# Kernel optimization log

Measured on AMD Instinct MI355X. Metric: run time of the kernel, lower is better.

Reference implementation:

```python
import jax, jax.numpy as jnp
import numpy as np


def _l2_normalize(x):
    # matches features.div(features.norm(2, 1, keepdim=True))
    return x / jnp.linalg.norm(x, ord=2, axis=1, keepdims=True)


def setup_inputs() -> dict:
    key = jax.random.key(0)
    k1, k2, k3 = jax.random.split(key, 3)
    B, N, D, C = 2048, 100000, 512, 1000
    return {
        "features": jax.random.normal(k1, (B, D), dtype=jnp.float32),
        "logits": jax.random.normal(k2, (B, C), dtype=jnp.float32),
        "db_features": jax.random.normal(k3, (N, D), dtype=jnp.float32),
        "k": 10,
    }


def reference(features, logits, db_features, k):
    # fit(): index.add(normalize(db_features)) -- faiss IndexFlatL2 stores rows
    xb = _l2_normalize(db_features)            # [N, D]
    # forward(): search normalized queries, take k-th (largest of the k) squared L2 dist
    xq = _l2_normalize(features)               # [B, D]
    # squared L2 distances via the expansion ||q||^2 + ||x||^2 - 2 q.x (faiss IndexFlatL2
    # returns SQUARED distances)
    q2 = jnp.sum(xq * xq, axis=1, keepdims=True)           # [B, 1]
    x2 = jnp.sum(xb * xb, axis=1)                          # [N]
    d2 = q2 + x2[None, :] - 2.0 * (xq @ xb.T)              # [B, N]
    # k smallest distances == k largest of -d2
    neg_topk, _ = jax.lax.top_k(-d2, k)                    # [B, k], sorted descending
    kth = -neg_topk[:, -1]                                 # k-th nearest squared distance
    return kth.reshape(-1, 1)
```

## Files before the change

### kernel.cpp

```cpp
#include <hip/hip_runtime.h>
#include <hip/hip_bf16.h>

typedef unsigned short ushort_t;
typedef unsigned char uchar_t;
typedef __attribute__((ext_vector_type(4))) int int4v;
typedef __attribute__((ext_vector_type(2))) unsigned int uint2v;

#define NQ      2048
#define ND      512
#define NDB     100000
#define TOPK    10
#define NCHUNK  98
#define CHUNK_N 1024
#define NPAD    (NCHUNK * CHUNK_N)
#define QTILES  (NQ / 128)
#define NTILES  (CHUNK_N / 128)
#define NWG     (NCHUNK * QTILES)
#define PERXCD  (NWG / 8)
#define QSCALE  400.0f
#define QINV    (1.0f / (QSCALE * QSCALE))
#define IMIN    (-2147483647 - 1)

#define GL2LDS(gp, lp) __builtin_amdgcn_global_load_lds(                      \
    (const __attribute__((address_space(1))) void*)(gp),                     \
    (__attribute__((address_space(3))) void*)(lp), 16, 0, 0)

__global__ void normalize_rows_i8(const float* __restrict__ in, uchar_t* __restrict__ out,
                                  int nvalid, int ntotal) {
    int row  = blockIdx.x * 4 + (threadIdx.x >> 6);
    int lane = threadIdx.x & 63;
    if (row >= ntotal) return;
    uint2v pk;
    if (row >= nvalid) {
        pk[0] = 0u; pk[1] = 0u;
    } else {
        const float4* src = reinterpret_cast<const float4*>(in + (size_t)row * ND);
        float4 v0 = src[lane * 2];
        float4 v1 = src[lane * 2 + 1];
        float s = v0.x*v0.x + v0.y*v0.y + v0.z*v0.z + v0.w*v0.w
                + v1.x*v1.x + v1.y*v1.y + v1.z*v1.z + v1.w*v1.w;
        #pragma unroll
        for (int off = 32; off; off >>= 1) s += __shfl_xor(s, off, 64);
        float r = rsqrtf(s) * QSCALE;
        float f[8] = { v0.x, v0.y, v0.z, v0.w, v1.x, v1.y, v1.z, v1.w };
        unsigned b[8];
        #pragma unroll
        for (int i = 0; i < 8; ++i) {
            int q = (int)rintf(f[i] * r);
            q = q > 127 ? 127 : (q < -127 ? -127 : q);
            b[i] = (unsigned)q & 0xFFu;
        }
        pk[0] = b[0] | (b[1] << 8) | (b[2] << 16) | (b[3] << 24);
        pk[1] = b[4] | (b[5] << 8) | (b[6] << 16) | (b[7] << 24);
    }
    *reinterpret_cast<uint2v*>(out + (size_t)row * ND + lane * 8) = pk;
}

__device__ inline void topk_insert_i(int (&top)[TOPK], int x) {
    #pragma unroll
    for (int i = 0; i < TOPK; ++i) {
        int mx = top[i] > x ? top[i] : x;
        int mn = top[i] > x ? x : top[i];
        top[i] = mx;
        x = mn;
    }
}

__global__ __launch_bounds__(256, 4)
void knn_chunk(const uchar_t* __restrict__ qb, const uchar_t* __restrict__ dbb,
               int* __restrict__ partial) {
    const int logical = (blockIdx.x & 7) * PERXCD + (blockIdx.x >> 3);
    const int qt = logical & (QTILES - 1);
    const int nc = logical >> 4;
    const int t = threadIdx.x, lane = t & 63, wv = t >> 6;

    __shared__ __align__(16) uchar_t As[128 * 64];
    __shared__ __align__(16) uchar_t Bs[128 * 64];

    int top[2][TOPK];
    #pragma unroll
    for (int qs = 0; qs < 2; ++qs)
        #pragma unroll
        for (int i = 0; i < TOPK; ++i) top[qs][i] = IMIN;

    const size_t nchunkbase = (size_t)nc * CHUNK_N;
    const int cb = wv * 128;
    const uchar_t* aseg = qb + (size_t)(qt * 128) * ND;

    int soff[2], doff[2];
    #pragma unroll
    for (int i = 0; i < 2; ++i) {
        const int cid = cb + i * 64 + lane;
        const int row = cid >> 2;
        const int c   = (cid & 3) ^ ((row >> 1) & 3);
        soff[i] = row * ND + c * 16;
        doff[i] = cid * 16;
    }
    const int cgrp = lane >> 4;
    int aoff[2];
    #pragma unroll
    for (int qs = 0; qs < 2; ++qs) {
        const int ar = wv * 32 + qs * 16 + (lane & 15);
        aoff[qs] = ar * 64 + ((cgrp ^ ((ar >> 1) & 3)) * 16);
    }
    int boff[8];
    #pragma unroll
    for (int ns = 0; ns < 8; ++ns) {
        const int br = ns * 16 + (lane & 15);
        boff[ns] = br * 64 + ((cgrp ^ ((br >> 1) & 3)) * 16);
    }

    for (int nt = 0; nt < NTILES; ++nt) {
        const uchar_t* bseg = dbb + (nchunkbase + nt * 128) * ND;
        int4v acc[2][8];
        #pragma unroll
        for (int a = 0; a < 2; ++a)
            #pragma unroll
            for (int b = 0; b < 8; ++b)
                acc[a][b] = (int4v){0, 0, 0, 0};

        #pragma unroll
        for (int ks = 0; ks < 8; ++ks) {
            const int kbase = ks * 64;
            __syncthreads();
            #pragma unroll
            for (int i = 0; i < 2; ++i) {
                GL2LDS(aseg + soff[i] + kbase, As + doff[i]);
                GL2LDS(bseg + soff[i] + kbase, Bs + doff[i]);
            }
            __syncthreads();
            int4v af[2], bf[8];
            #pragma unroll
            for (int qs = 0; qs < 2; ++qs)
                af[qs] = *reinterpret_cast<const int4v*>(As + aoff[qs]);
            #pragma unroll
            for (int ns = 0; ns < 8; ++ns)
                bf[ns] = *reinterpret_cast<const int4v*>(Bs + boff[ns]);
            #pragma unroll
            for (int qs = 0; qs < 2; ++qs)
                #pragma unroll
                for (int ns = 0; ns < 8; ++ns)
                    acc[qs][ns] = __builtin_amdgcn_mfma_i32_16x16x64_i8(bf[ns], af[qs], acc[qs][ns], 0, 0, 0);
        }

        #pragma unroll
        for (int qs = 0; qs < 2; ++qs) {
            int m = acc[qs][0][0];
            #pragma unroll
            for (int ns = 0; ns < 8; ++ns)
                #pragma unroll
                for (int r = 0; r < 4; ++r)
                    m = m > acc[qs][ns][r] ? m : acc[qs][ns][r];
            if (m > top[qs][TOPK - 1]) {
                #pragma unroll
                for (int ns = 0; ns < 8; ++ns)
                    #pragma unroll
                    for (int r = 0; r < 4; ++r) {
                        int v = acc[qs][ns][r];
                        if (v > top[qs][TOPK - 1]) topk_insert_i(top[qs], v);
                    }
            }
        }
    }

    #pragma unroll
    for (int qs = 0; qs < 2; ++qs) {
        #pragma unroll
        for (int step = 16; step <= 32; step <<= 1) {
            int other[TOPK];
            #pragma unroll
            for (int i = 0; i < TOPK; ++i) other[i] = __shfl_xor(top[qs][i], step, 64);
            #pragma unroll
            for (int i = 0; i < TOPK; ++i)
                if (other[i] > top[qs][TOPK - 1]) topk_insert_i(top[qs], other[i]);
        }
    }

    if ((lane >> 4) == 0) {
        #pragma unroll
        for (int qs = 0; qs < 2; ++qs) {
            const int q = qt * 128 + wv * 32 + qs * 16 + lane;
            int* dst = partial + ((size_t)nc * NQ + q) * TOPK;
            #pragma unroll
            for (int i = 0; i < TOPK; ++i) dst[i] = top[qs][i];
        }
    }
}

__global__ void final_merge(const int* __restrict__ partial, float* __restrict__ out) {
    const int q = blockIdx.x * 4 + (threadIdx.x >> 6);
    const int lane = threadIdx.x & 63;
    if (q >= NQ) return;
    int top[TOPK];
    #pragma unroll
    for (int i = 0; i < TOPK; ++i) top[i] = IMIN;
    for (int c = lane; c < NCHUNK; c += 64) {
        const int* p = partial + ((size_t)c * NQ + q) * TOPK;
        #pragma unroll
        for (int i = 0; i < TOPK; ++i) {
            int x = p[i];
            if (x > top[TOPK - 1]) topk_insert_i(top, x);
        }
    }
    #pragma unroll
    for (int step = 1; step <= 32; step <<= 1) {
        int other[TOPK];
        #pragma unroll
        for (int i = 0; i < TOPK; ++i) other[i] = __shfl_xor(top[i], step, 64);
        #pragma unroll
        for (int i = 0; i < TOPK; ++i)
            if (other[i] > top[TOPK - 1]) topk_insert_i(top, other[i]);
    }
    if (lane == 0) out[q] = 2.0f - 2.0f * ((float)top[TOPK - 1] * QINV);
}

extern "C" void kernel_launch(void* const* d_in, const int* in_sizes, int n_in,
                              void* d_out, int out_size, void* d_ws, size_t ws_size,
                              hipStream_t stream) {
    const float* features = (const float*)d_in[0];
    const float* dbf      = (const float*)d_in[2];
    float* out = (float*)d_out;

    uchar_t* dbb = (uchar_t*)d_ws;
    uchar_t* qbn = dbb + (size_t)NPAD * ND;
    int* partial = (int*)(qbn + (size_t)NQ * ND);

    normalize_rows_i8<<<NPAD / 4, 256, 0, stream>>>(dbf, dbb, NDB, NPAD);
    normalize_rows_i8<<<NQ / 4, 256, 0, stream>>>(features, qbn, NQ, NQ);
    knn_chunk<<<NWG, 256, 0, stream>>>(qbn, dbb, partial);
    final_merge<<<NQ / 4, 256, 0, stream>>>(partial, out);
}
```

Baseline: 327.1 us.

## Split knn tile across 8 waves, one 16-query slab per wave

```diff
diff --git a/kernel.cpp b/kernel.cpp
--- a/kernel.cpp
+++ b/kernel.cpp
@@ -66,124 +66,102 @@
     }
 }
 
-__global__ __launch_bounds__(256, 4)
+__global__ __launch_bounds__(512, 8)
 void knn_chunk(const uchar_t* __restrict__ qb, const uchar_t* __restrict__ dbb,
                int* __restrict__ partial) {
     const int logical = (blockIdx.x & 7) * PERXCD + (blockIdx.x >> 3);
     const int qt = logical & (QTILES - 1);
     const int nc = logical >> 4;
     const int t = threadIdx.x, lane = t & 63, wv = t >> 6;
+    const int l15 = lane & 15;
 
     __shared__ __align__(16) uchar_t As[128 * 64];
     __shared__ __align__(16) uchar_t Bs[128 * 64];
 
-    int top[2][TOPK];
-    #pragma unroll
-    for (int qs = 0; qs < 2; ++qs)
-        #pragma unroll
-        for (int i = 0; i < TOPK; ++i) top[qs][i] = IMIN;
+    int top[TOPK];
+    #pragma unroll
+    for (int i = 0; i < TOPK; ++i) top[i] = IMIN;
 
     const size_t nchunkbase = (size_t)nc * CHUNK_N;
-    const int cb = wv * 128;
     const uchar_t* aseg = qb + (size_t)(qt * 128) * ND;
 
-    int soff[2], doff[2];
-    #pragma unroll
-    for (int i = 0; i < 2; ++i) {
-        const int cid = cb + i * 64 + lane;
-        const int row = cid >> 2;
-        const int c   = (cid & 3) ^ ((row >> 1) & 3);
-        soff[i] = row * ND + c * 16;
-        doff[i] = cid * 16;
-    }
+    const int srow = t >> 2;
+    const int scol = (t & 3) ^ ((srow >> 1) & 3);
+    const int soff = srow * ND + scol * 16;
+    const int doff = t * 16;
     const int cgrp = lane >> 4;
-    int aoff[2];
-    #pragma unroll
-    for (int qs = 0; qs < 2; ++qs) {
-        const int ar = wv * 32 + qs * 16 + (lane & 15);
-        aoff[qs] = ar * 64 + ((cgrp ^ ((ar >> 1) & 3)) * 16);
-    }
-    int boff[8];
-    #pragma unroll
-    for (int ns = 0; ns < 8; ++ns) {
-        const int br = ns * 16 + (lane & 15);
-        boff[ns] = br * 64 + ((cgrp ^ ((br >> 1) & 3)) * 16);
-    }
+    const int slot = (cgrp ^ ((l15 >> 1) & 3)) * 16;
+    const int aoff = (wv * 16 + l15) * 64 + slot;
+    const int boff = l15 * 64 + slot;
 
     for (int nt = 0; nt < NTILES; ++nt) {
         const uchar_t* bseg = dbb + (nchunkbase + nt * 128) * ND;
-        int4v acc[2][8];
-        #pragma unroll
-        for (int a = 0; a < 2; ++a)
-            #pragma unroll
-            for (int b = 0; b < 8; ++b)
-                acc[a][b] = (int4v){0, 0, 0, 0};
+        int4v acc[8];
+        #pragma unroll
+        for (int b = 0; b < 8; ++b) acc[b] = (int4v){0, 0, 0, 0};
 
         #pragma unroll
         for (int ks = 0; ks < 8; ++ks) {
             const int kbase = ks * 64;
             __syncthreads();
+            GL2LDS(aseg + soff + kbase, As + doff);
+            GL2LDS(bseg + soff + kbase, Bs + doff);
+            __syncthreads();
+            int4v af = *reinterpret_cast<const int4v*>(As + aoff);
+            {
+                int4v bf0 = *reinterpret_cast<const int4v*>(Bs + boff);
+                int4v bf1 = *reinterpret_cast<const int4v*>(Bs + boff + 1024);
+                int4v bf2 = *reinterpret_cast<const int4v*>(Bs + boff + 2048);
+                int4v bf3 = *reinterpret_cast<const int4v*>(Bs + boff + 3072);
+                acc[0] = __builtin_amdgcn_mfma_i32_16x16x64_i8(bf0, af, acc[0], 0, 0, 0);
+                acc[1] = __builtin_amdgcn_mfma_i32_16x16x64_i8(bf1, af, acc[1], 0, 0, 0);
+                acc[2] = __builtin_amdgcn_mfma_i32_16x16x64_i8(bf2, af, acc[2], 0, 0, 0);
+                acc[3] = __builtin_amdgcn_mfma_i32_16x16x64_i8(bf3, af, acc[3], 0, 0, 0);
+            }
+            {
+                int4v bf4 = *reinterpret_cast<const int4v*>(Bs + boff + 4096);
+                int4v bf5 = *reinterpret_cast<const int4v*>(Bs + boff + 5120);
+                int4v bf6 = *reinterpret_cast<const int4v*>(Bs + boff + 6144);
+                int4v bf7 = *reinterpret_cast<const int4v*>(Bs + boff + 7168);
+                acc[4] = __builtin_amdgcn_mfma_i32_16x16x64_i8(bf4, af, acc[4], 0, 0, 0);
+                acc[5] = __builtin_amdgcn_mfma_i32_16x16x64_i8(bf5, af, acc[5], 0, 0, 0);
+                acc[6] = __builtin_amdgcn_mfma_i32_16x16x64_i8(bf6, af, acc[6], 0, 0, 0);
+                acc[7] = __builtin_amdgcn_mfma_i32_16x16x64_i8(bf7, af, acc[7], 0, 0, 0);
+            }
+        }
+
+        int m = acc[0][0];
+        #pragma unroll
+        for (int ns = 0; ns < 8; ++ns)
             #pragma unroll
-            for (int i = 0; i < 2; ++i) {
-                GL2LDS(aseg + soff[i] + kbase, As + doff[i]);
-                GL2LDS(bseg + soff[i] + kbase, Bs + doff[i]);
-            }
-            __syncthreads();
-            int4v af[2], bf[8];
-            #pragma unroll
-            for (int qs = 0; qs < 2; ++qs)
-                af[qs] = *reinterpret_cast<const int4v*>(As + aoff[qs]);
-            #pragma unroll
-            for (int ns = 0; ns < 8; ++ns)
-                bf[ns] = *reinterpret_cast<const int4v*>(Bs + boff[ns]);
-            #pragma unroll
-            for (int qs = 0; qs < 2; ++qs)
-                #pragma unroll
-                for (int ns = 0; ns < 8; ++ns)
-                    acc[qs][ns] = __builtin_amdgcn_mfma_i32_16x16x64_i8(bf[ns], af[qs], acc[qs][ns], 0, 0, 0);
-        }
-
-        #pragma unroll
-        for (int qs = 0; qs < 2; ++qs) {
-            int m = acc[qs][0][0];
+            for (int r = 0; r < 4; ++r)
+                m = m > acc[ns][r] ? m : acc[ns][r];
+        if (m > top[TOPK - 1]) {
             #pragma unroll
             for (int ns = 0; ns < 8; ++ns)
                 #pragma unroll
-                for (int r = 0; r < 4; ++r)
-                    m = m > acc[qs][ns][r] ? m : acc[qs][ns][r];
-            if (m > top[qs][TOPK - 1]) {
-                #pragma unroll
-                for (int ns = 0; ns < 8; ++ns)
-                    #pragma unroll
-                    for (int r = 0; r < 4; ++r) {
-                        int v = acc[qs][ns][r];
-                        if (v > top[qs][TOPK - 1]) topk_insert_i(top[qs], v);
-                    }
-            }
-        }
-    }
-
-    #pragma unroll
-    for (int qs = 0; qs < 2; ++qs) {
-        #pragma unroll
-        for (int step = 16; step <= 32; step <<= 1) {
-            int other[TOPK];
-            #pragma unroll
-            for (int i = 0; i < TOPK; ++i) other[i] = __shfl_xor(top[qs][i], step, 64);
-            #pragma unroll
-            for (int i = 0; i < TOPK; ++i)
-                if (other[i] > top[qs][TOPK - 1]) topk_insert_i(top[qs], other[i]);
-        }
+                for (int r = 0; r < 4; ++r) {
+                    int v = acc[ns][r];
+                    if (v > top[TOPK - 1]) topk_insert_i(top, v);
+                }
+        }
+    }
+
+    #pragma unroll
+    for (int step = 16; step <= 32; step <<= 1) {
+        int other[TOPK];
+        #pragma unroll
+        for (int i = 0; i < TOPK; ++i) other[i] = __shfl_xor(top[i], step, 64);
+        #pragma unroll
+        for (int i = 0; i < TOPK; ++i)
+            if (other[i] > top[TOPK - 1]) topk_insert_i(top, other[i]);
     }
 
     if ((lane >> 4) == 0) {
-        #pragma unroll
-        for (int qs = 0; qs < 2; ++qs) {
-            const int q = qt * 128 + wv * 32 + qs * 16 + lane;
-            int* dst = partial + ((size_t)nc * NQ + q) * TOPK;
-            #pragma unroll
-            for (int i = 0; i < TOPK; ++i) dst[i] = top[qs][i];
-        }
+        const int q = qt * 128 + wv * 16 + l15;
+        int* dst = partial + ((size_t)nc * NQ + q) * TOPK;
+        #pragma unroll
+        for (int i = 0; i < TOPK; ++i) dst[i] = top[i];
     }
 }
 
@@ -227,6 +205,6 @@
 
     normalize_rows_i8<<<NPAD / 4, 256, 0, stream>>>(dbf, dbb, NDB, NPAD);
     normalize_rows_i8<<<NQ / 4, 256, 0, stream>>>(features, qbn, NQ, NQ);
-    knn_chunk<<<NWG, 256, 0, stream>>>(qbn, dbb, partial);
+    knn_chunk<<<NWG, 512, 0, stream>>>(qbn, dbb, partial);
     final_merge<<<NQ / 4, 256, 0, stream>>>(partial, out);
 }
```

Measured after the change: 301.6 us. 1.08x faster.
